# Kernel optimization log

Measured on AMD Instinct MI355X. Metric: run time of the kernel, lower is better.

The kernel has to match this reference:

```python
import jax, jax.numpy as jnp
import numpy as np

N_HEADS = 16
N_KV_HEADS = 4
N_EMBED = 2048
HEAD_DIM = 128
SECTIONS = [16, 24, 24, 16, 24, 24]


def _process_rotary(c):
    # c: [3, B, T, HEAD_DIM] -> [B, 1, T, HEAD_DIM]
    splits = np.cumsum(SECTIONS)[:-1]
    secs = jnp.split(c, splits, axis=-1)
    out = jnp.concatenate([s[i % 3] for i, s in enumerate(secs)], axis=-1)
    return out[:, None]  # add head axis


def _rotate_half(x):
    x1, x2 = jnp.split(x, 2, axis=-1)
    return jnp.concatenate([-x2, x1], axis=-1)


def setup_inputs() -> dict:
    key = jax.random.key(0)
    ks = jax.random.split(key, 12)
    B, T = 1, 2048
    s = 0.02
    return {
        "x": jax.random.normal(ks[0], (B, T, N_EMBED), jnp.float32),
        "cos": jax.random.uniform(ks[1], (3, B, T, HEAD_DIM), jnp.float32),
        "sin": jax.random.uniform(ks[2], (3, B, T, HEAD_DIM), jnp.float32),
        "Wq": jax.random.normal(ks[3], (N_EMBED, N_EMBED), jnp.float32) * s,
        "bq": jax.random.normal(ks[4], (N_EMBED,), jnp.float32) * s,
        "Wk": jax.random.normal(ks[5], (N_EMBED, N_KV_HEADS * HEAD_DIM), jnp.float32) * s,
        "bk": jax.random.normal(ks[6], (N_KV_HEADS * HEAD_DIM,), jnp.float32) * s,
        "Wv": jax.random.normal(ks[7], (N_EMBED, N_KV_HEADS * HEAD_DIM), jnp.float32) * s,
        "bv": jax.random.normal(ks[8], (N_KV_HEADS * HEAD_DIM,), jnp.float32) * s,
        "Wo": jax.random.normal(ks[9], (N_EMBED, N_EMBED), jnp.float32) * s,
    }


def reference(x, cos, sin, Wq, bq, Wk, bk, Wv, bv, Wo):
    B, T, C = x.shape
    H, Hkv, D = N_HEADS, N_KV_HEADS, HEAD_DIM
    q = (x @ Wq + bq).reshape(B, T, H, D).transpose(0, 2, 1, 3)    # [B,H,T,D]
    k = (x @ Wk + bk).reshape(B, T, Hkv, D).transpose(0, 2, 1, 3)  # [B,Hkv,T,D]
    v = (x @ Wv + bv).reshape(B, T, Hkv, D).transpose(0, 2, 1, 3)
    # multi-section rope (cos/sin are 4-dim -> custom path)
    c = _process_rotary(cos)
    s = _process_rotary(sin)
    q = q * c + _rotate_half(q) * s
    k = k * c + _rotate_half(k) * s
    present_k, present_v = k, v
    # GQA expansion (repeat_interleave over head axis)
    r = H // Hkv
    k = jnp.repeat(k, r, axis=1)
    v = jnp.repeat(v, r, axis=1)
    # causal SDPA
    scores = jnp.einsum("bhqd,bhkd->bhqk", q, k) / jnp.sqrt(jnp.float32(D))
    causal = jnp.tril(jnp.ones((T, T), dtype=bool))
    scores = jnp.where(causal, scores, jnp.finfo(scores.dtype).min)
    attn = jax.nn.softmax(scores, axis=-1)
    y = jnp.einsum("bhqk,bhkd->bhqd", attn, v)
    y = y.transpose(0, 2, 1, 3).reshape(B, T, C)
    y = y @ Wo
    return (y, present_k, present_v)
```

## Files before the change

### kernel.cpp

```cpp
#include <hip/hip_runtime.h>

typedef unsigned short u16;
typedef unsigned int u32;
typedef __attribute__((ext_vector_type(4))) float f32x4;
typedef __attribute__((ext_vector_type(8))) __bf16 bf16x8;
typedef __attribute__((ext_vector_type(4))) u16 u16x4;
typedef __attribute__((ext_vector_type(2))) u32 u32x2;


__device__ __forceinline__ u16 f2bf(float f) {
  union { float f; unsigned u; } v; v.f = f;
  unsigned r = v.u + 0x7fffu + ((v.u >> 16) & 1u);
  return (u16)(r >> 16);
}

__device__ __forceinline__ u32 pack_bf2(float a, float b) {
  union { float f; unsigned u; } x, y;
  x.f = a; y.f = b;
#if __has_builtin(__builtin_amdgcn_perm)
  return __builtin_amdgcn_perm(y.u + 0x8000u, x.u + 0x8000u, 0x07060302u);
#else
  return (u32)((x.u + 0x8000u) >> 16) | ((y.u + 0x8000u) & 0xffff0000u);
#endif
}

__device__ __forceinline__ void stage16(const void* g, void* l) {
#if __has_builtin(__builtin_amdgcn_global_load_lds)
  __builtin_amdgcn_global_load_lds((const __attribute__((address_space(1))) void*)g,
                                   (__attribute__((address_space(3))) void*)l, 16, 0, 0);
#else
  *(f32x4*)l = *(const f32x4*)g;
#endif
}

__device__ __forceinline__ f32x4 mfma16(bf16x8 a, bf16x8 b, f32x4 c) {
  return __builtin_amdgcn_mfma_f32_16x16x32_bf16(a, b, c, 0, 0, 0);
}

__device__ __forceinline__ float fexp2(float x) {
#if __has_builtin(__builtin_amdgcn_exp2f)
  return __builtin_amdgcn_exp2f(x);
#else
  return exp2f(x);
#endif
}

__device__ __forceinline__ int rope_ch(int d) {
  int dd = (d < 64) ? d : d - 64;
  return (dd < 16) ? 0 : (dd < 40 ? 1 : 2);
}


__global__ void yuna_prep(const float* __restrict__ x, u16* __restrict__ xb,
                          const float* __restrict__ cosp, const float* __restrict__ sinp,
                          float* __restrict__ csel, float* __restrict__ ssel,
                          const float* __restrict__ Wq, const float* __restrict__ Wk,
                          const float* __restrict__ Wv, const float* __restrict__ Wo,
                          u16* __restrict__ Wb, u16* __restrict__ Wob) {
  __shared__ float tile[64][65];
  const int bid = blockIdx.x;
  if (bid < 4096) {
    const int mat = bid >> 10;
    const int rem = bid & 1023;
    const float* W;
    u16* out;
    int N;
    if (mat == 0)      { W = Wq; out = Wb;                          N = 2048; }
    else if (mat == 1) { W = Wk; out = Wb + (size_t)2048 * 2048;    N = 512; }
    else if (mat == 2) { W = Wv; out = Wb + (size_t)2560 * 2048;    N = 512; }
    else               { W = Wo; out = Wob;                         N = 2048; }
    int k0 = (rem & 31) << 6, n0 = (rem >> 5) << 6;
    if (n0 >= N) return;
    int tx = threadIdx.x & 63, ty = threadIdx.x >> 6;
#pragma unroll
    for (int j = 0; j < 64; j += 4)
      tile[ty + j][tx] = W[(size_t)(k0 + ty + j) * N + n0 + tx];
    __syncthreads();
#pragma unroll
    for (int j = 0; j < 64; j += 4)
      out[(size_t)(n0 + ty + j) * 2048 + k0 + tx] = f2bf(tile[tx][ty + j]);
  } else if (bid < 8192) {
    int i = (bid - 4096) * 256 + threadIdx.x;
    f32x4 v = ((const f32x4*)x)[i];
    u16x4 o;
    o.x = f2bf(v.x); o.y = f2bf(v.y); o.z = f2bf(v.z); o.w = f2bf(v.w);
    ((u16x4*)xb)[i] = o;
  } else {
    int i = (bid - 8192) * 256 + threadIdx.x;
    int i4 = i * 4;
    int t = i4 >> 7, d = i4 & 127;
    f32x4 c, s;
#pragma unroll
    for (int j = 0; j < 4; ++j) {
      int ch = rope_ch(d + j);
      c[j] = cosp[(size_t)ch * 262144 + (size_t)t * 128 + d + j];
      s[j] = sinp[(size_t)ch * 262144 + (size_t)t * 128 + d + j];
    }
    ((f32x4*)csel)[i] = c;
    ((f32x4*)ssel)[i] = s;
  }
}

__global__ __launch_bounds__(256, 3) void yuna_gemm_qkv(
    const u16* __restrict__ A, const u16* __restrict__ Bt,
    const float* __restrict__ bq, const float* __restrict__ bk, const float* __restrict__ bv,
    const float* __restrict__ csel, const float* __restrict__ ssel,
    u16* __restrict__ qb, u16* __restrict__ kb, u16* __restrict__ vtb,
    float* __restrict__ pk, float* __restrict__ pv) {
  const int K = 2048;
  __shared__ __align__(16) char smem[49152];
  const int tid = threadIdx.x;
  const int wave = tid >> 6, lane = tid & 63;
  const int lrow = lane & 15, lkg = lane >> 4;
  const int m0 = blockIdx.x * 64;
  const int by = blockIdx.y;
  const int n0 = by * 128;
  const int sw = lrow & 7;

  const int srow = tid >> 3;
  const int ssc = (tid & 7) ^ ((tid >> 3) & 7);
  const size_t abase = (size_t)(m0 + srow) * K + ssc * 8;
  const size_t bbase = (size_t)(n0 + srow) * K + ssc * 8;

  const f32x4 fzero = {0.f, 0.f, 0.f, 0.f};
  f32x4 acc[4][2];
#pragma unroll
  for (int mi = 0; mi < 4; ++mi) { acc[mi][0] = fzero; acc[mi][1] = fzero; }

#pragma unroll
  for (int it = 0; it < 2; ++it)
    stage16(A + abase + (size_t)it * 32 * K, smem + (tid + it * 256) * 16);
#pragma unroll
  for (int it = 0; it < 4; ++it)
    stage16(Bt + bbase + (size_t)it * 32 * K, smem + 16384 + (tid + it * 256) * 16);

  for (int k0 = 0, ki = 0; k0 < K; k0 += 64, ++ki) {
    const int cur = ki & 1;
    const char* Asb = smem + cur * 8192;
    const char* Bsb = smem + 16384 + cur * 16384;
    if (k0 + 64 < K) {
      char* Asn = smem + (cur ^ 1) * 8192;
      char* Bsn = smem + 16384 + (cur ^ 1) * 16384;
#pragma unroll
      for (int it = 0; it < 2; ++it)
        stage16(A + abase + (size_t)it * 32 * K + k0 + 64, Asn + (tid + it * 256) * 16);
#pragma unroll
      for (int it = 0; it < 4; ++it)
        stage16(Bt + bbase + (size_t)it * 32 * K + k0 + 64, Bsn + (tid + it * 256) * 16);
      asm volatile("s_waitcnt vmcnt(6)\n\ts_barrier" ::: "memory");
    } else {
      asm volatile("s_waitcnt vmcnt(0)\n\ts_barrier" ::: "memory");
    }
#pragma unroll
    for (int kk = 0; kk < 2; ++kk) {
      const int cof = ((kk * 4 + lkg) ^ sw) << 4;
      bf16x8 af[4], bfr[2];
#pragma unroll
      for (int mi = 0; mi < 4; ++mi)
        af[mi] = *(const bf16x8*)(Asb + (mi * 16 + lrow) * 128 + cof);
#pragma unroll
      for (int ni = 0; ni < 2; ++ni)
        bfr[ni] = *(const bf16x8*)(Bsb + (wave * 16 + ni * 64 + lrow) * 128 + cof);
#pragma unroll
      for (int mi = 0; mi < 4; ++mi)
#pragma unroll
        for (int ni = 0; ni < 2; ++ni)
          acc[mi][ni] = mfma16(af[mi], bfr[ni], acc[mi][ni]);
    }
    asm volatile("s_barrier" ::: "memory");
  }

  if (by >= 20) {
    const int kvh = by - 20;
#pragma unroll
    for (int mi = 0; mi < 4; ++mi)
#pragma unroll
      for (int ni = 0; ni < 2; ++ni) {
        int d = wave * 16 + ni * 64 + lrow;
        float bb = bv[kvh * 128 + d];
        int mb = mi * 16 + lkg * 4;
        float v0 = acc[mi][ni][0] + bb, v1 = acc[mi][ni][1] + bb;
        float v2 = acc[mi][ni][2] + bb, v3 = acc[mi][ni][3] + bb;
        size_t pb = ((size_t)(kvh * 2048 + m0 + mb)) * 128 + d;
        pv[pb] = v0; pv[pb + 128] = v1; pv[pb + 256] = v2; pv[pb + 384] = v3;
        u16x4 w;
        w.x = f2bf(v0); w.y = f2bf(v1); w.z = f2bf(v2); w.w = f2bf(v3);
        *(u16x4*)(vtb + ((size_t)(kvh * 128 + d)) * 2048 + m0 + mb) = w;
      }
  } else {
    const float QSCALE = 1.4426950408889634f * 0.08838834764831845f;
    const bool isQ = (by < 16);
    const int h = isQ ? by : (by - 16);
    const float* bias = isQ ? bq : bk;
    const int dlo = wave * 16 + lrow;
    const float blo = bias[h * 128 + dlo];
    const float bhi = bias[h * 128 + dlo + 64];
#pragma unroll
    for (int mi = 0; mi < 4; ++mi) {
      const int tb = m0 + mi * 16 + lkg * 4;
#pragma unroll
      for (int r = 0; r < 4; ++r) {
        const int t = tb + r;
        float a = acc[mi][0][r] + blo;
        float b = acc[mi][1][r] + bhi;
        size_t cb = (size_t)t * 128 + dlo;
        float cl = csel[cb], sl = ssel[cb];
        float ch = csel[cb + 64], sh = ssel[cb + 64];
        float lo = a * cl - b * sl;
        float hi = b * ch + a * sh;
        size_t o = (((size_t)(h * 2048 + t)) << 7) + dlo;
        if (isQ) {
          qb[o] = f2bf(lo * QSCALE);
          qb[o + 64] = f2bf(hi * QSCALE);
        } else {
          kb[o] = f2bf(lo);
          kb[o + 64] = f2bf(hi);
          pk[o] = lo; pk[o + 64] = hi;
        }
      }
    }
  }
}

__global__ __launch_bounds__(256, 3) void yuna_gemm_out(
    const u16* __restrict__ A, const u16* __restrict__ Bt, float* __restrict__ C) {
  const int K = 2048;
  __shared__ __align__(16) char smem[49152];
  const int tid = threadIdx.x;
  const int wave = tid >> 6, lane = tid & 63;
  const int lrow = lane & 15, lkg = lane >> 4;
  const int m0 = blockIdx.x * 64;
  const int n0 = blockIdx.y * 128;
  const int wc = wave * 32;
  const int sw = lrow & 7;

  const int srow = tid >> 3;
  const int ssc = (tid & 7) ^ ((tid >> 3) & 7);
  const size_t abase = (size_t)(m0 + srow) * K + ssc * 8;
  const size_t bbase = (size_t)(n0 + srow) * K + ssc * 8;

  const f32x4 fzero = {0.f, 0.f, 0.f, 0.f};
  f32x4 acc[4][2];
#pragma unroll
  for (int mi = 0; mi < 4; ++mi) { acc[mi][0] = fzero; acc[mi][1] = fzero; }

#pragma unroll
  for (int it = 0; it < 2; ++it)
    stage16(A + abase + (size_t)it * 32 * K, smem + (tid + it * 256) * 16);
#pragma unroll
  for (int it = 0; it < 4; ++it)
    stage16(Bt + bbase + (size_t)it * 32 * K, smem + 16384 + (tid + it * 256) * 16);

  for (int k0 = 0, ki = 0; k0 < K; k0 += 64, ++ki) {
    const int cur = ki & 1;
    const char* Asb = smem + cur * 8192;
    const char* Bsb = smem + 16384 + cur * 16384;
    if (k0 + 64 < K) {
      char* Asn = smem + (cur ^ 1) * 8192;
      char* Bsn = smem + 16384 + (cur ^ 1) * 16384;
#pragma unroll
      for (int it = 0; it < 2; ++it)
        stage16(A + abase + (size_t)it * 32 * K + k0 + 64, Asn + (tid + it * 256) * 16);
#pragma unroll
      for (int it = 0; it < 4; ++it)
        stage16(Bt + bbase + (size_t)it * 32 * K + k0 + 64, Bsn + (tid + it * 256) * 16);
      asm volatile("s_waitcnt vmcnt(6)\n\ts_barrier" ::: "memory");
    } else {
      asm volatile("s_waitcnt vmcnt(0)\n\ts_barrier" ::: "memory");
    }
#pragma unroll
    for (int kk = 0; kk < 2; ++kk) {
      const int cof = ((kk * 4 + lkg) ^ sw) << 4;
      bf16x8 af[4], bfr[2];
#pragma unroll
      for (int mi = 0; mi < 4; ++mi)
        af[mi] = *(const bf16x8*)(Asb + (mi * 16 + lrow) * 128 + cof);
#pragma unroll
      for (int ni = 0; ni < 2; ++ni)
        bfr[ni] = *(const bf16x8*)(Bsb + (wc + ni * 16 + lrow) * 128 + cof);
#pragma unroll
      for (int mi = 0; mi < 4; ++mi)
#pragma unroll
        for (int ni = 0; ni < 2; ++ni)
          acc[mi][ni] = mfma16(af[mi], bfr[ni], acc[mi][ni]);
    }
    asm volatile("s_barrier" ::: "memory");
  }
#pragma unroll
  for (int mi = 0; mi < 4; ++mi)
#pragma unroll
    for (int ni = 0; ni < 2; ++ni) {
      int d = wc + ni * 16 + lrow;
      int mb = mi * 16 + lkg * 4;
#pragma unroll
      for (int r = 0; r < 4; ++r)
        C[(size_t)(m0 + mb + r) * 2048 + n0 + d] = acc[mi][ni][r];
    }
}

__global__ __launch_bounds__(256, 2) void yuna_flash_attn(
    const u16* __restrict__ Q,
    const u16* __restrict__ Kb,
    const u16* __restrict__ Vt,
    float* __restrict__ OpA,
    float* __restrict__ OpB,
    float* __restrict__ ml) {
  __shared__ __align__(16) u16 Ks[2][64 * 128];
  __shared__ __align__(16) u16 Vs[2][128 * 64];
  __shared__ __align__(16) u16 Ps[64 * 64];
  const int h = blockIdx.x;
  const int yb = blockIdx.y;
  const int qb = 31 - (yb >> 1);
  const int half = yb & 1;
  const int ca = (qb + 2) >> 1;
  const int kb0 = half ? ca : 0;
  const int kb1 = half ? (qb + 1) : ca;
  const int kvh = h >> 2;
  const int tid = threadIdx.x, wave = tid >> 6, lane = tid & 63;
  const int lrow = lane & 15, lkg = lane >> 4;
  const int m = wave * 16 + lrow;
  const int sw = lrow & 7;
  const int qglob = qb * 64 + m;

  const int krow = tid >> 4;
  const int ksc = (tid & 15) ^ ((tid >> 4) & 7);
  const size_t kbase0 = ((size_t)(kvh * 2048 + krow) << 7) + ksc * 8;
  const int vrow = tid >> 3;
  const int vsc = (tid & 7) ^ ((tid >> 3) & 7);
  const size_t vbase0 = (size_t)(kvh * 128 + vrow) * 2048 + vsc * 8;

  bf16x8 qf[4];
#pragma unroll
  for (int kk = 0; kk < 4; ++kk)
    qf[kk] = *(const bf16x8*)(Q + (((size_t)h * 2048 + qglob) << 7) + kk * 32 + lkg * 8);

  const f32x4 fzero = {0.f, 0.f, 0.f, 0.f};
  f32x4 o[8];
#pragma unroll
  for (int dt = 0; dt < 8; ++dt) o[dt] = fzero;
  float m_i = -1e30f, l_i = 0.f;

  if (kb0 < kb1) {
#pragma unroll
    for (int it = 0; it < 4; ++it)
      stage16(Kb + kbase0 + ((size_t)(kb0 * 64 + it * 16) << 7), (char*)Ks[0] + (tid + it * 256) * 16);
#pragma unroll
    for (int it = 0; it < 4; ++it)
      stage16(Vt + vbase0 + (size_t)it * 32 * 2048 + kb0 * 64, (char*)Vs[0] + (tid + it * 256) * 16);

    for (int kb = kb0; kb < kb1; ++kb) {
      const int cur = (kb - kb0) & 1;
      const char* Ksb = (const char*)Ks[cur];
      const char* Vsb = (const char*)Vs[cur];
      if (kb + 1 < kb1) {
        char* Ksn = (char*)Ks[cur ^ 1];
        char* Vsn = (char*)Vs[cur ^ 1];
#pragma unroll
        for (int it = 0; it < 4; ++it)
          stage16(Kb + kbase0 + ((size_t)((kb + 1) * 64 + it * 16) << 7), Ksn + (tid + it * 256) * 16);
#pragma unroll
        for (int it = 0; it < 4; ++it)
          stage16(Vt + vbase0 + (size_t)it * 32 * 2048 + (kb + 1) * 64, Vsn + (tid + it * 256) * 16);
        asm volatile("s_waitcnt vmcnt(8)\n\ts_barrier" ::: "memory");
      } else {
        asm volatile("s_waitcnt vmcnt(0)\n\ts_barrier" ::: "memory");
      }

      f32x4 s[4];
#pragma unroll
      for (int nt = 0; nt < 4; ++nt) s[nt] = fzero;
      __builtin_amdgcn_s_setprio(1);
#pragma unroll
      for (int kk = 0; kk < 4; ++kk) {
        const int cof = ((kk * 4 + lkg) ^ sw) << 4;
        bf16x8 kf[4];
#pragma unroll
        for (int nt = 0; nt < 4; ++nt)
          kf[nt] = *(const bf16x8*)(Ksb + (nt * 16 + lrow) * 256 + cof);
#pragma unroll
        for (int nt = 0; nt < 4; ++nt)
          s[nt] = mfma16(kf[nt], qf[kk], s[nt]);
      }
      __builtin_amdgcn_s_setprio(0);
      if (kb == qb) {
        const int kbase = kb * 64 + lkg * 4;
#pragma unroll
        for (int nt = 0; nt < 4; ++nt)
#pragma unroll
          for (int r = 0; r < 4; ++r)
            if (kbase + nt * 16 + r > qglob) s[nt][r] = -1e30f;
      }

      float mx = -1e30f;
#pragma unroll
      for (int nt = 0; nt < 4; ++nt)
#pragma unroll
        for (int r = 0; r < 4; ++r) mx = fmaxf(mx, s[nt][r]);
      mx = fmaxf(mx, __shfl_xor(mx, 16));
      mx = fmaxf(mx, __shfl_xor(mx, 32));
      if (__any(mx > m_i + 8.0f)) {
        float mnew = fmaxf(m_i, mx);
        float alpha = fexp2(m_i - mnew);
        m_i = mnew;
        l_i *= alpha;
#pragma unroll
        for (int dt = 0; dt < 8; ++dt) o[dt] *= alpha;
      }
      float ps = 0.f;
      const int hh = lkg & 1;
#pragma unroll
      for (int nt = 0; nt < 4; ++nt) {
        float p0 = fexp2(s[nt][0] - m_i);
        float p1 = fexp2(s[nt][1] - m_i);
        float p2 = fexp2(s[nt][2] - m_i);
        float p3 = fexp2(s[nt][3] - m_i);
        ps += (p0 + p1) + (p2 + p3);
        u32x2 pk2;
        pk2.x = pack_bf2(p0, p1);
        pk2.y = pack_bf2(p2, p3);
        int cc = 2 * nt + (lkg >> 1);
        *(u32x2*)((char*)Ps + m * 128 + ((cc ^ (m & 7)) << 4) + hh * 8) = pk2;
      }
      l_i += ps;

      __builtin_amdgcn_s_setprio(1);
#pragma unroll
      for (int kk = 0; kk < 2; ++kk) {
        const int cof = ((kk * 4 + lkg) ^ sw) << 4;
        bf16x8 pf = *(const bf16x8*)((char*)Ps + m * 128 + cof);
        bf16x8 vf[8];
#pragma unroll
        for (int dt = 0; dt < 8; ++dt)
          vf[dt] = *(const bf16x8*)(Vsb + (dt * 16 + lrow) * 128 + cof);
#pragma unroll
        for (int dt = 0; dt < 8; ++dt)
          o[dt] = mfma16(vf[dt], pf, o[dt]);
      }
      __builtin_amdgcn_s_setprio(0);
      asm volatile("s_barrier" ::: "memory");
    }
  }

  l_i += __shfl_xor(l_i, 16);
  l_i += __shfl_xor(l_i, 32);
  size_t row = (size_t)h * 2048 + qglob;
  if (lkg == 0)
    *(float2*)(ml + ((size_t)(half << 15) + row) * 2) = float2{m_i, l_i};
  float* orow = (half ? OpB : OpA) + row * 128 + lkg * 4;
#pragma unroll
  for (int dt = 0; dt < 8; ++dt)
    *(f32x4*)(orow + dt * 16) = o[dt];
}

__global__ void yuna_merge(const float* __restrict__ OpA, const float* __restrict__ OpB,
                           const float* __restrict__ ml, u16* __restrict__ Y) {
  int idx = blockIdx.x * 256 + threadIdx.x;
  int d4 = idx & 31;
  int t = (idx >> 5) & 2047;
  int h = idx >> 16;
  size_t row = (size_t)h * 2048 + t;
  float2 a2 = *(const float2*)(ml + row * 2);
  float2 b2 = *(const float2*)(ml + (32768 + row) * 2);
  float M = fmaxf(a2.x, b2.x);
  float wA = fexp2(a2.x - M), wB = fexp2(b2.x - M);
  float inv = 1.f / (a2.y * wA + b2.y * wB);
  wA *= inv; wB *= inv;
  f32x4 a = ((const f32x4*)OpA)[row * 32 + d4];
  f32x4 b = ((const f32x4*)OpB)[row * 32 + d4];
  u16x4 w;
  w.x = f2bf(a[0] * wA + b[0] * wB);
  w.y = f2bf(a[1] * wA + b[1] * wB);
  w.z = f2bf(a[2] * wA + b[2] * wB);
  w.w = f2bf(a[3] * wA + b[3] * wB);
  *(u16x4*)(Y + (size_t)t * 2048 + h * 128 + d4 * 4) = w;
}


extern "C" void kernel_launch(void* const* d_in, const int* in_sizes, int n_in,
                              void* d_out, int out_size, void* d_ws, size_t ws_size,
                              hipStream_t stream) {
  const float* x = (const float*)d_in[0];
  const float* cosp = (const float*)d_in[1];
  const float* sinp = (const float*)d_in[2];
  const float* Wq = (const float*)d_in[3];
  const float* bq = (const float*)d_in[4];
  const float* Wk = (const float*)d_in[5];
  const float* bk = (const float*)d_in[6];
  const float* Wv = (const float*)d_in[7];
  const float* bv = (const float*)d_in[8];
  const float* Wo = (const float*)d_in[9];
  float* out = (float*)d_out;
  float* out_k = out + 4194304;
  float* out_v = out + 5242880;

  char* ws = (char*)d_ws;
  u16* xb   = (u16*)(ws + 0);
  u16* Wb   = (u16*)(ws + 8388608);
  u16* Wob  = (u16*)(ws + 20971520);
  float* csel = (float*)(ws + 29360128);
  float* ssel = (float*)(ws + 30408704);
  u16* qbuf = (u16*)(ws + 54525952);
  u16* kbuf = (u16*)(ws + 62914560);
  u16* vtb  = (u16*)(ws + 65011712);
  u16* yat  = (u16*)(ws + 67108864);
  float* opA = (float*)(ws + 0);
  float* mlb = (float*)(ws + 17825792);
  float* opB = (float*)(ws + 31457280);

  yuna_prep<<<8448, 256, 0, stream>>>(x, xb, cosp, sinp, csel, ssel,
                                      Wq, Wk, Wv, Wo, Wb, Wob);
  yuna_gemm_qkv<<<dim3(32, 24), 256, 0, stream>>>(xb, Wb, bq, bk, bv, csel, ssel,
                                                  qbuf, kbuf, vtb, out_k, out_v);
  yuna_flash_attn<<<dim3(16, 64), 256, 0, stream>>>(qbuf, kbuf, vtb, opA, opB, mlb);
  yuna_merge<<<4096, 256, 0, stream>>>(opA, opB, mlb, yat);
  yuna_gemm_out<<<dim3(32, 16), 256, 0, stream>>>(yat, Wob, out);
}
```

Baseline: 216.9 us.

## Split KV only for long query blocks; finalize short blocks directly in attention

Query blocks 16-31, the longer causal rows, keep the two-way KV split with partial outputs. Blocks 0-15 now run unsplit, normalize their output in-kernel, and write bf16 Y through an LDS transpose. The merge kernel shrinks to cover only the upper half of query rows. This removes fp32 partial writes and merge work for short rows, at the cost of a longer critical path for unsplit blocks and fewer total blocks (48 vs 64 per head).

```diff
diff --git a/kernel.cpp b/kernel.cpp
--- a/kernel.cpp
+++ b/kernel.cpp
@@ -304,17 +304,27 @@
     const u16* __restrict__ Vt,
     float* __restrict__ OpA,
     float* __restrict__ OpB,
-    float* __restrict__ ml) {
+    float* __restrict__ ml,
+    u16* __restrict__ Y) {
   __shared__ __align__(16) u16 Ks[2][64 * 128];
   __shared__ __align__(16) u16 Vs[2][128 * 64];
   __shared__ __align__(16) u16 Ps[64 * 64];
   const int h = blockIdx.x;
   const int yb = blockIdx.y;
-  const int qb = 31 - (yb >> 1);
-  const int half = yb & 1;
-  const int ca = (qb + 2) >> 1;
-  const int kb0 = half ? ca : 0;
-  const int kb1 = half ? (qb + 1) : ca;
+  int qb, kb0, kb1, half;
+  if (yb < 32) {
+    qb = 31 - (yb >> 1);
+    half = yb & 1;
+    int ca = (qb + 2) >> 1;
+    kb0 = half ? ca : 0;
+    kb1 = half ? (qb + 1) : ca;
+  } else {
+    qb = 47 - yb;
+    half = 0;
+    kb0 = 0;
+    kb1 = qb + 1;
+  }
+  const bool split = (yb < 32);
   const int kvh = h >> 2;
   const int tid = threadIdx.x, wave = tid >> 6, lane = tid & 63;
   const int lrow = lane & 15, lkg = lane >> 4;
@@ -340,7 +350,7 @@
   for (int dt = 0; dt < 8; ++dt) o[dt] = fzero;
   float m_i = -1e30f, l_i = 0.f;
 
-  if (kb0 < kb1) {
+  {
 #pragma unroll
     for (int it = 0; it < 4; ++it)
       stage16(Kb + kbase0 + ((size_t)(kb0 * 64 + it * 16) << 7), (char*)Ks[0] + (tid + it * 256) * 16);
@@ -443,21 +453,45 @@
 
   l_i += __shfl_xor(l_i, 16);
   l_i += __shfl_xor(l_i, 32);
-  size_t row = (size_t)h * 2048 + qglob;
-  if (lkg == 0)
-    *(float2*)(ml + ((size_t)(half << 15) + row) * 2) = float2{m_i, l_i};
-  float* orow = (half ? OpB : OpA) + row * 128 + lkg * 4;
-#pragma unroll
-  for (int dt = 0; dt < 8; ++dt)
-    *(f32x4*)(orow + dt * 16) = o[dt];
+  if (split) {
+    size_t row = (size_t)h * 2048 + qglob;
+    if (lkg == 0)
+      *(float2*)(ml + ((size_t)(half << 15) + row) * 2) = float2{m_i, l_i};
+    float* orow = (half ? OpB : OpA) + row * 128 + lkg * 4;
+#pragma unroll
+    for (int dt = 0; dt < 8; ++dt)
+      *(f32x4*)(orow + dt * 16) = o[dt];
+  } else {
+    __syncthreads();
+    {
+      float inv = 1.f / l_i;
+      const int hh = lkg & 1;
+#pragma unroll
+      for (int dt = 0; dt < 8; ++dt) {
+        u32x2 w2;
+        w2.x = pack_bf2(o[dt][0] * inv, o[dt][1] * inv);
+        w2.y = pack_bf2(o[dt][2] * inv, o[dt][3] * inv);
+        int cc = 2 * dt + (lkg >> 1);
+        *(u32x2*)((char*)Ks + m * 256 + ((cc ^ (m & 7)) << 4) + hh * 8) = w2;
+      }
+    }
+    __syncthreads();
+#pragma unroll
+    for (int it = 0; it < 4; ++it) {
+      int c = tid + it * 256;
+      int row = c >> 4, cc = c & 15;
+      f32x4 v = *(const f32x4*)((const char*)Ks + row * 256 + ((cc ^ (row & 7)) << 4));
+      *(f32x4*)(Y + (size_t)(qb * 64 + row) * 2048 + h * 128 + cc * 8) = v;
+    }
+  }
 }
 
 __global__ void yuna_merge(const float* __restrict__ OpA, const float* __restrict__ OpB,
                            const float* __restrict__ ml, u16* __restrict__ Y) {
   int idx = blockIdx.x * 256 + threadIdx.x;
   int d4 = idx & 31;
-  int t = (idx >> 5) & 2047;
-  int h = idx >> 16;
+  int t = 1024 + ((idx >> 5) & 1023);
+  int h = idx >> 15;
   size_t row = (size_t)h * 2048 + t;
   float2 a2 = *(const float2*)(ml + row * 2);
   float2 b2 = *(const float2*)(ml + (32768 + row) * 2);
@@ -511,7 +545,7 @@
                                       Wq, Wk, Wv, Wo, Wb, Wob);
   yuna_gemm_qkv<<<dim3(32, 24), 256, 0, stream>>>(xb, Wb, bq, bk, bv, csel, ssel,
                                                   qbuf, kbuf, vtb, out_k, out_v);
-  yuna_flash_attn<<<dim3(16, 64), 256, 0, stream>>>(qbuf, kbuf, vtb, opA, opB, mlb);
-  yuna_merge<<<4096, 256, 0, stream>>>(opA, opB, mlb, yat);
+  yuna_flash_attn<<<dim3(16, 48), 256, 0, stream>>>(qbuf, kbuf, vtb, opA, opB, mlb, yat);
+  yuna_merge<<<2048, 256, 0, stream>>>(opA, opB, mlb, yat);
   yuna_gemm_out<<<dim3(32, 16), 256, 0, stream>>>(yat, Wob, out);
 }
```

Measured after the change: 223.8 us. 3.2% more time.
